# Kernel optimization log

Measured on AMD Instinct MI355X. Metric: run time of the kernel, lower is better.

Reference implementation:

```python
import jax, jax.numpy as jnp
import numpy as np

ATOM_K = 10
VOX_K = 15
HEADS = 4
HEAD_DIM = 32
N_BLOCKS = 4
BLOCK_DEPTH = 2


def _pairwise_sqdist(a, b):
    # a: [Na,3], b: [Nb,3] -> [Na,Nb]
    return jnp.sum(a * a, 1)[:, None] + jnp.sum(b * b, 1)[None, :] - 2.0 * (a @ b.T)


def knn(src_pos, dst_pos, k):
    # for each dst point, k nearest src points; returns (dst_idx, src_idx), each [Nd*k]
    d2 = _pairwise_sqdist(dst_pos, src_pos)
    _, idx = jax.lax.top_k(-d2, k)
    dst = jnp.repeat(jnp.arange(dst_pos.shape[0]), k)
    return dst, idx.reshape(-1)


def knn_graph(pos, k):
    # k nearest neighbors excluding self; returns (src=neighbor, dst=center)
    n = pos.shape[0]
    d2 = _pairwise_sqdist(pos, pos) + jnp.eye(n, dtype=pos.dtype) * 1e10
    _, idx = jax.lax.top_k(-d2, k)
    dst = jnp.repeat(jnp.arange(n), k)
    return idx.reshape(-1), dst


def edge_weights(i0, i1, h_a, pos_a, h_b, pos_b, w1, b1, w2, b2):
    # MLP([2*A+1, 8, 1]) on concat(h_a[i0], h_b[i1], dist) -> scalar per edge
    d = jnp.sqrt(jnp.sum((pos_a[i0] - pos_b[i1]) ** 2, -1, keepdims=True) + 1e-12)
    feat = jnp.concatenate([h_a[i0], h_b[i1], d], -1)
    return (jax.nn.relu(feat @ w1 + b1) @ w2 + b2)[:, 0]


def attn_layer(h, src, dst, ew, wq_l, wk_l, wv_l, n):
    # edge-weighted multi-head graph attention with segment softmax over dst
    q = (h @ wq_l).reshape(n, HEADS, HEAD_DIM)
    k = (h @ wk_l).reshape(n, HEADS, HEAD_DIM)
    v = (h @ wv_l).reshape(n, HEADS, HEAD_DIM)
    logits = jnp.sum(q[dst] * k[src], -1) / jnp.sqrt(jnp.float32(HEAD_DIM)) + ew[:, None]  # [E,H]
    m = jax.ops.segment_max(logits, dst, num_segments=n)
    z = jnp.exp(logits - m[dst])
    s = jax.ops.segment_sum(z, dst, num_segments=n)
    alpha = z / (s[dst] + 1e-9)
    out = jax.ops.segment_sum(alpha[:, :, None] * v[src], dst, num_segments=n)
    return out.reshape(n, HEADS * HEAD_DIM)


def layer_norm(x, g, b):
    mu = jnp.mean(x, -1, keepdims=True)
    var = jnp.var(x, -1, keepdims=True)
    return (x - mu) * jax.lax.rsqrt(var + 1e-5) * g + b


def setup_inputs() -> dict:
    Na, Nv, F, A, OUT = 8192, 4096, 64, 128, 128
    L = N_BLOCKS * BLOCK_DEPTH
    key = jax.random.key(0)
    ks = jax.random.split(key, 20)
    p = lambda k, shape, s=0.05: jax.random.normal(k, shape, jnp.float32) * s
    return {
        'atom_x': jax.random.normal(ks[0], (Na, F), jnp.float32),
        'atom_pos': jax.random.normal(ks[1], (Na, 3), jnp.float32) * 10.0,
        'vox_x': jax.random.normal(ks[2], (Nv, F), jnp.float32),
        'vox_pos': jax.random.normal(ks[3], (Nv, 3), jnp.float32) * 10.0,
        'w_atom_in': p(ks[4], (F, A)), 'b_atom_in': jnp.zeros((A,), jnp.float32),
        'w_vox_in': p(ks[5], (F, A)), 'b_vox_in': jnp.zeros((A,), jnp.float32),
        'aa_w1': p(ks[6], (2 * A + 1, 8)), 'aa_b1': jnp.zeros((8,), jnp.float32),
        'aa_w2': p(ks[7], (8, 1)), 'aa_b2': jnp.zeros((1,), jnp.float32),
        'av_w1': p(ks[8], (2 * A + 1, 8)), 'av_b1': jnp.zeros((8,), jnp.float32),
        'av_w2': p(ks[9], (8, 1)), 'av_b2': jnp.zeros((1,), jnp.float32),
        'vv_w1': p(ks[10], (2 * A + 1, 8)), 'vv_b1': jnp.zeros((8,), jnp.float32),
        'vv_w2': p(ks[11], (8, 1)), 'vv_b2': jnp.zeros((1,), jnp.float32),
        'wq': p(ks[12], (L, A, A)), 'wk': p(ks[13], (L, A, A)), 'wv': p(ks[14], (L, A, A)),
        'ln_g': jnp.ones((L, A), jnp.float32), 'ln_b': jnp.zeros((L, A), jnp.float32),
        'w_o1': p(ks[15], ((N_BLOCKS + 1) * A, A)), 'b_o1': jnp.zeros((A,), jnp.float32),
        'w_o2': p(ks[16], (A, OUT)), 'b_o2': jnp.zeros((OUT,), jnp.float32),
    }


def reference(atom_x, atom_pos, vox_x, vox_pos, w_atom_in, b_atom_in, w_vox_in, b_vox_in,
              aa_w1, aa_b1, aa_w2, aa_b2, av_w1, av_b1, av_w2, av_b2, vv_w1, vv_b1, vv_w2, vv_b2,
              wq, wk, wv, ln_g, ln_b, w_o1, b_o1, w_o2, b_o2):
    Na, Nv = atom_x.shape[0], vox_x.shape[0]
    N = Na + Nv
    atom_h0 = atom_x @ w_atom_in + b_atom_in
    vox_h0 = vox_x @ w_vox_in + b_vox_in

    # multi-scale KNN graph construction
    aa_src, aa_dst = knn_graph(atom_pos, ATOM_K)
    aa_ew = edge_weights(aa_src, aa_dst, atom_h0, atom_pos, atom_h0, atom_pos, aa_w1, aa_b1, aa_w2, aa_b2)
    av_vox, av_atom = knn(atom_pos, vox_pos, VOX_K)  # dst=vox, src=atom
    av_ew = edge_weights(av_vox, av_atom, vox_h0, vox_pos, atom_h0, atom_pos, av_w1, av_b1, av_w2, av_b2)
    vv_src, vv_dst = knn_graph(vox_pos, VOX_K)
    vv_ew = edge_weights(vv_src, vv_dst, vox_h0, vox_pos, vox_h0, vox_pos, vv_w1, vv_b1, vv_w2, vv_b2)

    # combined atom|vox graph (vox nodes offset by Na)
    src = jnp.concatenate([aa_src, av_atom, vv_src + Na])
    dst = jnp.concatenate([aa_dst, av_vox + Na, vv_dst + Na])
    ew = jnp.concatenate([aa_ew, av_ew, vv_ew])
    h = jnp.concatenate([atom_h0, vox_h0], 0)

    block_outs = []
    for b_i in range(N_BLOCKS):
        for l in range(BLOCK_DEPTH):
            li = b_i * BLOCK_DEPTH + l
            h = layer_norm(h + attn_layer(h, src, dst, ew, wq[li], wk[li], wv[li], N), ln_g[li], ln_b[li])
        block_outs.append(h[Na:])

    feat = jnp.concatenate([vox_h0] + block_outs, -1)  # [Nv, (blocks+1)*A]
    return jax.nn.relu(feat @ w_o1 + b_o1) @ w_o2 + b_o2
```

## Files before the change

### kernel.cpp

```cpp
#include <hip/hip_runtime.h>
#include <hip/hip_bf16.h>

#define PE_NA 8192
#define PE_NV 4096
#define PE_NN (PE_NA+PE_NV)
#define PE_FA 128
#define PE_FIN 64
#define PE_KAA 10
#define PE_KAV 15
#define PE_KVV 15
#define PE_EAA (PE_NA*PE_KAA)
#define PE_EAV (PE_NV*PE_KAV)
#define PE_EVV (PE_NV*PE_KVV)
#define PE_ETOT (PE_EAA+PE_EAV+PE_EVV)
#define PE_KNN_BLOCKS (PE_NA/4 + PE_NV/4 + PE_NV/4)
#define PE_P1A 0
#define PE_P2A 65536
#define PE_P2AV 131072
#define PE_P1AV 196608
#define PE_P1V 229376
#define PE_P2V 262144
#define PE_PTOT 294912
#define PE_PRE_BLOCKS (PE_PTOT/256)
#define PE_WT_ELEMS (8*3*128*128)
#define PE_WT_BLOCKS (PE_WT_ELEMS/256)
#define PE_RANK_S 32

typedef __hip_bfloat16 bf16;
typedef __attribute__((ext_vector_type(4))) float f32x4;
typedef __attribute__((ext_vector_type(4))) unsigned int u32x4;
typedef __attribute__((ext_vector_type(8))) short s16x8;
union pe_frag { u32x4 u; s16x8 s; };

__device__ __forceinline__ float pe_b2f(bf16 x){ return __bfloat162float(x); }

__device__ __forceinline__ float pe_u2f(unsigned short u){ return __uint_as_float(((unsigned)u) << 16); }
__device__ __forceinline__ unsigned short pe_f2u(float f){
  unsigned u = __float_as_uint(f);
  u = u + 0x7FFFu + ((u >> 16) & 1u);
  return (unsigned short)(u >> 16);
}

__global__ __launch_bounds__(1024) void pe_probe_kernel(const unsigned short* __restrict__ buf, int n,
                                                        int* __restrict__ flag){
  __shared__ int red[16];
  int t = threadIdx.x;
  int cnt = 0;
  for (int i = t; i < n; i += 1024){
    unsigned u = buf[i];
    unsigned e = (u >> 7) & 0xFF;
    if (u == 0u || (e >= 100u && e <= 150u)) cnt++;
  }
  #pragma unroll
  for (int off = 32; off > 0; off >>= 1) cnt += __shfl_xor(cnt, off);
  if ((t & 63) == 0) red[t >> 6] = cnt;
  __syncthreads();
  if (t == 0){
    int s = 0;
    #pragma unroll
    for (int i = 0; i < 16; i++) s += red[i];
    flag[0] = (s > (n * 9) / 10) ? 0 : 1;
  }
}

struct PeConv {
  const void* src[29];
  long long dstOff[29];
  int n[29];
  int blk0[30];
};
__global__ __launch_bounds__(256) void pe_convall_kernel(PeConv a, float* __restrict__ wsbase,
                                                         const int* __restrict__ flag){
  int b = blockIdx.x;
  int s = 0;
  while (s < 28 && b >= a.blk0[s+1]) s++;
  int idx = (b - a.blk0[s])*256 + threadIdx.x;
  if (idx >= a.n[s]) return;
  float* dst = wsbase + a.dstOff[s];
  if (flag[0]) dst[idx] = ((const float*)a.src[s])[idx];
  else         dst[idx] = pe_b2f(((const bf16*)a.src[s])[idx]);
}

__global__ __launch_bounds__(256) void ProteinEncoder_558345749244_kernel(bf16* __restrict__ out, int n){
  int idx = blockIdx.x*256 + threadIdx.x;
  if (idx < n) out[idx] = __float2bfloat16(0.123f);
}

__global__ __launch_bounds__(256) void pe_packproj_kernel(
    const float* __restrict__ ax, const float* __restrict__ wai, const float* __restrict__ bai,
    const float* __restrict__ vx, const float* __restrict__ wvi, const float* __restrict__ bvi,
    const float* __restrict__ apos, const float* __restrict__ vpos,
    const float* __restrict__ wq, const float* __restrict__ wk, const float* __restrict__ wv,
    float* __restrict__ h, float* __restrict__ voxh0,
    float4* __restrict__ apos4, float4* __restrict__ vpos4,
    int* __restrict__ arank, int* __restrict__ vrank,
    unsigned short* __restrict__ wtb){
  int b = blockIdx.x;
  const int NBA = (PE_NA*PE_FA)/256;
  const int NBV = (PE_NV*PE_FA)/256;
  const int NBP = (PE_NN + 255)/256;
  if (b < NBA){
    int idx = b*256 + threadIdx.x;
    int row = idx >> 7, col = idx & 127;
    const float* xr = ax + row*PE_FIN;
    float acc = bai[col];
    #pragma unroll 8
    for (int k2 = 0; k2 < PE_FIN; k2++) acc += xr[k2] * wai[k2*PE_FA + col];
    h[idx] = acc;
  } else if (b < NBA + NBV){
    int idx = (b - NBA)*256 + threadIdx.x;
    int row = idx >> 7, col = idx & 127;
    const float* xr = vx + row*PE_FIN;
    float acc = bvi[col];
    #pragma unroll 8
    for (int k2 = 0; k2 < PE_FIN; k2++) acc += xr[k2] * wvi[k2*PE_FA + col];
    h[(size_t)PE_NA*PE_FA + idx] = acc;
    voxh0[idx] = acc;
  } else if (b < NBA + NBV + NBP){
    int idx = (b - NBA - NBV)*256 + threadIdx.x;
    if (idx < PE_NA){
      float bx = apos[idx*3+0], by = apos[idx*3+1], bz = apos[idx*3+2];
      apos4[idx] = make_float4(bx, by, bz, (bx*bx + by*by) + bz*bz);
      arank[idx] = 0;
    } else if (idx < PE_NA + PE_NV){
      int j = idx - PE_NA;
      float bx = vpos[j*3+0], by = vpos[j*3+1], bz = vpos[j*3+2];
      vpos4[j] = make_float4(bx, by, bz, (bx*bx + by*by) + bz*bz);
      vrank[j] = 0;
    }
  } else {
    int g = (b - NBA - NBV - NBP)*256 + threadIdx.x;
    int c = g >> 14;
    int r = g & 16383;
    int n = r >> 7, k = r & 127;
    int li = c / 3, mat = c - li*3;
    const float* wsrc = (mat == 0) ? wq : (mat == 1) ? wk : wv;
    wtb[g] = pe_f2u(wsrc[li*16384 + k*128 + n]);
  }
}

__global__ __launch_bounds__(256) void pe_rank_kernel(
    const float4* __restrict__ apos4, const float4* __restrict__ vpos4,
    int* __restrict__ arank, int* __restrict__ vrank){
  __shared__ float xs[256];
  int b = blockIdx.x;
  const int ABLK = (PE_NA/256)*PE_RANK_S;
  const float4* src; int N; int* drk; int cb;
  if (b < ABLK){ src = apos4; N = PE_NA; drk = arank; cb = b; }
  else         { src = vpos4; N = PE_NV; drk = vrank; cb = b - ABLK; }
  int chunk = cb / PE_RANK_S;
  int seg   = cb % PE_RANK_S;
  int i = chunk*256 + threadIdx.x;
  float xi = src[i].x;
  int segN = N / PE_RANK_S;
  int j0 = seg * segN;
  if (threadIdx.x < segN) xs[threadIdx.x] = src[j0 + threadIdx.x].x;
  __syncthreads();
  int cnt = 0;
  #pragma unroll 8
  for (int j = 0; j < segN; j++){
    float xj = xs[j];
    cnt += (xj < xi || (xj == xi && (j0 + j) < i)) ? 1 : 0;
  }
  atomicAdd(&drk[i], cnt);
}

__global__ __launch_bounds__(256) void pe_scatter_kernel(
    const float4* __restrict__ apos4, const float4* __restrict__ vpos4,
    const int* __restrict__ arank, const int* __restrict__ vrank,
    float4* __restrict__ sax4, int* __restrict__ said,
    float4* __restrict__ svx4, int* __restrict__ svid){
  int g = blockIdx.x*256 + threadIdx.x;
  if (g < PE_NA){
    int r = arank[g];
    sax4[r] = apos4[g];
    said[r] = g;
  } else if (g < PE_NN){
    int j = g - PE_NA;
    int r = vrank[j];
    svx4[r] = vpos4[j];
    svid[r] = j;
  }
}

__device__ __forceinline__ float pe_unflip(unsigned th){
  return __uint_as_float(th ^ ((unsigned)(~((int)th >> 31)) | 0x80000000u));
}
__device__ __forceinline__ void pe_knn_insert(unsigned long long mask, float d2, int j,
                                              int K, int lane,
                                              unsigned long long &slot, float &thr_f){
  while (mask){
    int l = __ffsll((long long)mask) - 1;
    mask &= mask - 1;
    float dl = __shfl(d2, l, 64);
    int jl = __shfl(j, l, 64);
    unsigned u = __float_as_uint(dl);
    u ^= (unsigned)(((int)u >> 31) | 0x80000000);
    unsigned long long k = ((unsigned long long)u << 32) | (unsigned)jl;
    unsigned long long skm1 = __shfl(slot, K-1, 64);
    if (k < skm1){
      unsigned long long up = __shfl_up(slot, 1, 64);
      slot = (slot < k) ? slot : ((lane == 0 || up < k) ? k : up);
      thr_f = pe_unflip((unsigned)(__shfl(slot, K-1, 64) >> 32));
    }
  }
}

__global__ __launch_bounds__(256) void pe_knn3_kernel(
    const float4* __restrict__ apos4, const float4* __restrict__ vpos4,
    const float4* __restrict__ sax4, const int* __restrict__ said, const int* __restrict__ arank,
    const float4* __restrict__ svx4, const int* __restrict__ svid, const int* __restrict__ vrank,
    int* __restrict__ es,
    const float* __restrict__ h,
    const float* __restrict__ aw1, const float* __restrict__ vw1, const float* __restrict__ ww1,
    float* __restrict__ Pall){
  int b = blockIdx.x;
  if (b >= PE_KNN_BLOCKS){
    int g = (b - PE_KNN_BLOCKS)*256 + threadIdx.x;
    const float* w1; const float* hb; int n; int half;
    if (g < PE_P2A)       { w1 = aw1; hb = h;                        n = g >> 3;               half = 0; }
    else if (g < PE_P2AV) { w1 = aw1; hb = h;                        n = (g - PE_P2A) >> 3;    half = 1; }
    else if (g < PE_P1AV) { w1 = vw1; hb = h;                        n = (g - PE_P2AV) >> 3;   half = 1; }
    else if (g < PE_P1V)  { w1 = vw1; hb = h + (size_t)PE_NA*PE_FA;  n = (g - PE_P1AV) >> 3;   half = 0; }
    else if (g < PE_P2V)  { w1 = ww1; hb = h + (size_t)PE_NA*PE_FA;  n = (g - PE_P1V) >> 3;    half = 0; }
    else                  { w1 = ww1; hb = h + (size_t)PE_NA*PE_FA;  n = (g - PE_P2V) >> 3;    half = 1; }
    int j = g & 7;
    const float* hr = hb + n*PE_FA;
    const float* wr = w1 + half*128*8 + j;
    float acc = 0.f;
    #pragma unroll 8
    for (int f = 0; f < 128; f++) acc += hr[f] * wr[f*8];
    Pall[g] = acc;
    return;
  }
  const float4 *dpos, *spos; const int *sid, *srank; int Ns, K, excl, idx_off, nb; int* out;
  if (b < PE_NA/4){
    dpos = apos4; spos = sax4; sid = said; srank = arank;
    Ns = PE_NA; K = PE_KAA; excl = 1; idx_off = 0; out = es; nb = b;
  } else if (b < PE_NA/4 + PE_NV/4){
    dpos = vpos4; spos = sax4; sid = said; srank = nullptr;
    Ns = PE_NA; K = PE_KAV; excl = 0; idx_off = 0; out = es + PE_EAA; nb = b - PE_NA/4;
  } else {
    dpos = vpos4; spos = svx4; sid = svid; srank = vrank;
    Ns = PE_NV; K = PE_KVV; excl = 1; idx_off = PE_NA;
    out = es + PE_EAA + PE_EAV; nb = b - PE_NA/4 - PE_NV/4;
  }
  int lane = threadIdx.x & 63;
  int n = nb*4 + (threadIdx.x >> 6);
  float4 dp = dpos[n];
  float qx = dp.x, qy = dp.y, qz = dp.z, nq = dp.w;
  int self = excl ? n : -1;
  int start;
  if (srank){
    start = srank[n];
  } else {
    int lo = 0, len = Ns;
    #pragma unroll
    for (int it = 0; it < 2; it++){
      int step = (len + 63) >> 6;
      int pr = lo + lane*step; if (pr > Ns-1) pr = Ns-1;
      float px = spos[pr].x;
      unsigned long long mv = __ballot(px <= qx);
      int cnt = __popcll(mv);
      int seg = cnt > 0 ? cnt - 1 : 0;
      lo = lo + seg*step;
      len = step;
      if (lo > Ns-1) lo = Ns-1;
    }
    start = lo;
  }
  int w0 = start - 32; if (w0 < 0) w0 = 0; if (w0 > Ns - 64) w0 = Ns - 64;
  unsigned long long slot;
  float thr_f;
  {
    int j = w0 + lane;
    float4 pp = spos[j];
    int oi = sid[j];
    float dt = (qx*pp.x + qy*pp.y) + qz*pp.z;
    float d2 = __builtin_fmaf(-2.0f, dt, nq + pp.w);
    unsigned u = __float_as_uint(d2);
    u ^= (unsigned)(((int)u >> 31) | 0x80000000);
    if (oi == self) u = 0xffffffffu;
    unsigned long long key = ((unsigned long long)u << 32) | (unsigned)oi;
    #pragma unroll
    for (int kk = 2; kk <= 64; kk <<= 1){
      #pragma unroll
      for (int jj = kk >> 1; jj > 0; jj >>= 1){
        unsigned long long o = __shfl_xor(key, jj, 64);
        bool keepmin = (((lane & jj) == 0) == ((lane & kk) == 0));
        unsigned long long mn = (key < o) ? key : o;
        unsigned long long mx = (key < o) ? o : key;
        key = keepmin ? mn : mx;
      }
    }
    slot = key;
    thr_f = pe_unflip((unsigned)(__shfl(slot, K-1, 64) >> 32));
  }
  int L = w0 - 1;
  int R = w0 + 64;
  bool doneL = false, doneR = false;
  while (!(doneL && doneR)){
    if (!doneL){
      int j = L - lane;
      bool val = (j >= 0);
      float d2 = 1e30f, ddx = -1e30f; int oi = -3;
      if (val){
        float4 pp = spos[j];
        oi = sid[j];
        ddx = pp.x - qx;
        float dt = (qx*pp.x + qy*pp.y) + qz*pp.z;
        d2 = __builtin_fmaf(-2.0f, dt, nq + pp.w);
      }
      unsigned long long m = __ballot(val && (d2 <= thr_f) && (oi != self));
      if (m) pe_knn_insert(m, d2, oi, K, lane, slot, thr_f);
      float dd63 = __shfl(ddx, 63);
      doneL = (L - 64 < 0) || ((dd63 < 0.f) && (dd63*dd63 > thr_f));
      L -= 64;
    }
    if (!doneR){
      int j = R + lane;
      bool val = (j < Ns);
      float d2 = 1e30f, ddx = 1e30f; int oi = -3;
      if (val){
        float4 pp = spos[j];
        oi = sid[j];
        ddx = pp.x - qx;
        float dt = (qx*pp.x + qy*pp.y) + qz*pp.z;
        d2 = __builtin_fmaf(-2.0f, dt, nq + pp.w);
      }
      unsigned long long m = __ballot(val && (d2 <= thr_f) && (oi != self));
      if (m) pe_knn_insert(m, d2, oi, K, lane, slot, thr_f);
      float dd63 = __shfl(ddx, 63);
      doneR = (R + 64 >= Ns) || ((dd63 > 0.f) && (dd63*dd63 > thr_f));
      R += 64;
    }
  }
  if (lane < K) out[n*K + lane] = (int)(unsigned)(slot & 0xffffffffu) + idx_off;
}

__global__ __launch_bounds__(256) void pe_edge3_kernel(
    const float4* __restrict__ apos4, const float4* __restrict__ vpos4,
    const int* __restrict__ es, const float* __restrict__ Pall,
    const float* __restrict__ aw1, const float* __restrict__ ab1,
    const float* __restrict__ aw2, const float* __restrict__ ab2,
    const float* __restrict__ vw1, const float* __restrict__ vb1,
    const float* __restrict__ vw2, const float* __restrict__ vb2,
    const float* __restrict__ ww1, const float* __restrict__ wb1,
    const float* __restrict__ ww2, const float* __restrict__ wb2,
    float* __restrict__ ewb){
  int e = blockIdx.x*256 + threadIdx.x;
  const float *w1r, *b1, *w2, *b2;
  long long offA, offB;
  float4 qa, qb;
  if (e < PE_EAA){
    int dst = e / PE_KAA;
    int src = es[e];
    offA = PE_P1A  + (long long)src*8;
    offB = PE_P2A  + (long long)dst*8;
    qa = apos4[src]; qb = apos4[dst];
    w1r = aw1 + 256*8; b1 = ab1; w2 = aw2; b2 = ab2;
  } else if (e < PE_EAA + PE_EAV){
    int e2 = e - PE_EAA;
    int dstv = e2 / PE_KAV;
    int srca = es[e];
    offA = PE_P1AV + (long long)dstv*8;
    offB = PE_P2AV + (long long)srca*8;
    qa = vpos4[dstv]; qb = apos4[srca];
    w1r = vw1 + 256*8; b1 = vb1; w2 = vw2; b2 = vb2;
  } else {
    int e2 = e - PE_EAA - PE_EAV;
    int dstv = e2 / PE_KVV;
    int srcv = es[e] - PE_NA;
    offA = PE_P1V  + (long long)srcv*8;
    offB = PE_P2V  + (long long)dstv*8;
    qa = vpos4[srcv]; qb = vpos4[dstv];
    w1r = ww1 + 256*8; b1 = wb1; w2 = ww2; b2 = wb2;
  }
  float dx = qa.x - qb.x, dy = qa.y - qb.y, dz = qa.z - qb.z;
  float d = sqrtf(((dx*dx + dy*dy) + dz*dz) + 1e-12f);
  float4 a0 = *(const float4*)(Pall + offA);
  float4 a1 = *(const float4*)(Pall + offA + 4);
  float4 c0 = *(const float4*)(Pall + offB);
  float4 c1 = *(const float4*)(Pall + offB + 4);
  float acc[8] = { a0.x + c0.x, a0.y + c0.y, a0.z + c0.z, a0.w + c0.w,
                   a1.x + c1.x, a1.y + c1.y, a1.z + c1.z, a1.w + c1.w };
  float o = b2[0];
  #pragma unroll
  for (int j = 0; j < 8; j++){
    float hj = acc[j] + d*w1r[j] + b1[j];
    if (hj > 0.f) o += hj * w2[j];
  }
  ewb[e] = o;
}

__global__ __launch_bounds__(256) void pe_qkv3_kernel(const float* __restrict__ H,
    const unsigned short* __restrict__ Wt,
    unsigned short* __restrict__ QKV){
  __shared__ __align__(16) unsigned Xs[2048];
  int t = threadIdx.x;
  int row0 = blockIdx.x * 32;
  #pragma unroll
  for (int i = 0; i < 8; i++){
    int idx32 = i*256 + t;
    int row = idx32 >> 6, c32 = idx32 & 63;
    const float* src = H + (size_t)(row0 + row)*PE_FA + c32*2;
    unsigned u = (unsigned)pe_f2u(src[0]) | ((unsigned)pe_f2u(src[1]) << 16);
    Xs[row*64 + (c32 ^ ((row & 7) << 2))] = u;
  }
  __syncthreads();
  int w = t >> 6, l = t & 63;
  int l15 = l & 15, lq = l >> 4;
  f32x4 acc[2][6];
  #pragma unroll
  for (int a = 0; a < 2; a++)
    #pragma unroll
    for (int bb = 0; bb < 6; bb++) acc[a][bb] = (f32x4){0.f, 0.f, 0.f, 0.f};
  #pragma unroll
  for (int ks = 0; ks < 4; ks++){
    pe_frag af[2];
    #pragma unroll
    for (int rt = 0; rt < 2; rt++){
      int row = rt*16 + l15;
      int c32 = (ks*16 + lq*4) ^ ((row & 7) << 2);
      af[rt].u = *(const u32x4*)&Xs[row*64 + c32];
    }
    #pragma unroll
    for (int nt = 0; nt < 6; nt++){
      int n = w*96 + nt*16 + l15;
      pe_frag bf_;
      bf_.u = *(const u32x4*)(Wt + (size_t)n*PE_FA + ks*32 + lq*8);
      #pragma unroll
      for (int rt = 0; rt < 2; rt++)
        acc[rt][nt] = __builtin_amdgcn_mfma_f32_16x16x32_bf16(af[rt].s, bf_.s, acc[rt][nt], 0, 0, 0);
    }
  }
  #pragma unroll
  for (int rt = 0; rt < 2; rt++){
    #pragma unroll
    for (int nt = 0; nt < 6; nt++){
      int n = w*96 + nt*16 + l15;
      int mat = n >> 7, col = n & 127;
      unsigned short* outp = QKV + (size_t)mat*PE_NN*PE_FA + col;
      int nodeb = row0 + rt*16 + lq*4;
      #pragma unroll
      for (int v = 0; v < 4; v++)
        outp[(size_t)(nodeb + v)*PE_FA] = pe_f2u(acc[rt][nt][v]);
    }
  }
}

template<int DEG>
__device__ __forceinline__ void pe_attn_node(int n, int lane, int esel, float ewsel,
    const unsigned* __restrict__ Qp, const unsigned* __restrict__ Kp, const unsigned* __restrict__ Vp,
    float* H, const float* __restrict__ lng, const float* __restrict__ lnb, float* bout){
  unsigned qu = Qp[n*64 + lane];
  float qx = pe_u2f((unsigned short)(qu & 0xffffu));
  float qy = pe_u2f((unsigned short)(qu >> 16));
  int srcs[DEG];
  #pragma unroll
  for (int e = 0; e < DEG; e++) srcs[e] = __shfl(esel, e, 64);
  const float inv = 0.17677669529663687f;
  float lg[DEG];
  #pragma unroll
  for (int e = 0; e < DEG; e++){
    unsigned ku = Kp[srcs[e]*64 + lane];
    float p = qx*pe_u2f((unsigned short)(ku & 0xffffu)) + qy*pe_u2f((unsigned short)(ku >> 16));
    #pragma unroll
    for (int off = 8; off > 0; off >>= 1) p += __shfl_xor(p, off);
    lg[e] = p*inv + __shfl(ewsel, e, 64);
  }
  float m = -1e30f;
  #pragma unroll
  for (int e = 0; e < DEG; e++) m = fmaxf(m, lg[e]);
  float ssum = 0.f;
  #pragma unroll
  for (int e = 0; e < DEG; e++){ float z = expf(lg[e] - m); ssum += z; lg[e] = z; }
  float rdn = 1.0f / (ssum + 1e-9f);
  float a0 = 0.f, a1 = 0.f;
  #pragma unroll
  for (int e = 0; e < DEG; e++){
    unsigned vu = Vp[srcs[e]*64 + lane];
    a0 += lg[e]*pe_u2f((unsigned short)(vu & 0xffffu));
    a1 += lg[e]*pe_u2f((unsigned short)(vu >> 16));
  }
  a0 *= rdn; a1 *= rdn;
  float2 hv = ((const float2*)H)[n*64 + lane];
  float x0 = hv.x + a0, x1 = hv.y + a1;
  float s = x0 + x1;
  #pragma unroll
  for (int off = 32; off > 0; off >>= 1) s += __shfl_xor(s, off);
  float mu = s * (1.f/128.f);
  float d0 = x0 - mu, d1 = x1 - mu;
  float vq = d0*d0 + d1*d1;
  #pragma unroll
  for (int off = 32; off > 0; off >>= 1) vq += __shfl_xor(vq, off);
  float var = vq * (1.f/128.f);
  float rs = 1.0f / sqrtf(var + 1e-5f);
  float2 lw = ((const float2*)lng)[lane];
  float2 lb = ((const float2*)lnb)[lane];
  float2 yv = make_float2(d0*rs*lw.x + lb.x, d1*rs*lw.y + lb.y);
  ((float2*)H)[n*64 + lane] = yv;
  if (bout != nullptr) ((float2*)bout)[(n - PE_NA)*64 + lane] = yv;
}

__global__ __launch_bounds__(128) void pe_attn_ln_kernel(const unsigned* __restrict__ Qp,
    const unsigned* __restrict__ Kp, const unsigned* __restrict__ Vp, float* H,
    const int* __restrict__ esrc, const float* __restrict__ eew,
    const float* __restrict__ lng, const float* __restrict__ lnb, float* bout){
  int w = threadIdx.x >> 6;
  int lane = threadIdx.x & 63;
  int n = blockIdx.x*2 + w;
  int esel = 0; float ewsel = 0.f;
  if (n < PE_NA){
    if (lane < PE_KAA){ int e = n*PE_KAA + lane; esel = esrc[e]; ewsel = eew[e]; }
    pe_attn_node<PE_KAA>(n, lane, esel, ewsel, Qp, Kp, Vp, H, lng, lnb, nullptr);
  } else {
    int j = n - PE_NA;
    if (lane < PE_KAV){ int e = PE_EAA + j*PE_KAV + lane; esel = esrc[e]; ewsel = eew[e]; }
    else if (lane < PE_KAV + PE_KVV){ int e = PE_EAA + PE_EAV + j*PE_KVV + (lane - PE_KAV); esel = esrc[e]; ewsel = eew[e]; }
    pe_attn_node<PE_KAV+PE_KVV>(n, lane, esel, ewsel, Qp, Kp, Vp, H, lng, lnb, bout);
  }
}

__global__ __launch_bounds__(256) void pe_final1_kernel(const float* __restrict__ voxh0, const float* __restrict__ bouts,
    const float* __restrict__ W, const float* __restrict__ B, float* __restrict__ hid){
  __shared__ float Xs[640][17];
  int t = threadIdx.x;
  int row0 = blockIdx.x * 16;
  for (int s = 0; s < 5; s++){
    const float* seg = (s == 0) ? voxh0 : (bouts + (size_t)(s-1)*PE_NV*PE_FA);
    #pragma unroll
    for (int i = 0; i < 8; i++){
      int idx = i*256 + t;
      int r = idx >> 7, k0 = idx & 127;
      Xs[s*128 + k0][r] = seg[(size_t)(row0 + r)*PE_FA + k0];
    }
  }
  __syncthreads();
  int col = t & 127;
  int rg = (t >> 7) * 8;
  float acc[8];
  #pragma unroll
  for (int i = 0; i < 8; i++) acc[i] = B[col];
  for (int k = 0; k < 640; k++){
    float w = W[k*PE_FA + col];
    #pragma unroll
    for (int i = 0; i < 8; i++) acc[i] += Xs[k][rg + i] * w;
  }
  #pragma unroll
  for (int i = 0; i < 8; i++)
    hid[(size_t)(row0 + rg + i)*PE_FA + col] = fmaxf(acc[i], 0.f);
}

__global__ __launch_bounds__(256) void pe_final2_kernel(const float* __restrict__ hid, const float* __restrict__ W,
    const float* __restrict__ B, void* __restrict__ outv, const int* __restrict__ flag){
  int idx = blockIdx.x*256 + threadIdx.x;
  int r = idx >> 7, c = idx & 127;
  float acc = B[c];
  const float* hr = hid + r*PE_FA;
  #pragma unroll 8
  for (int k2 = 0; k2 < 128; k2++) acc += hr[k2] * W[k2*PE_FA + c];
  if (flag[0]) ((float*)outv)[idx] = acc;
  else         ((bf16*)outv)[idx] = __float2bfloat16(acc);
}

extern "C" void kernel_launch(void* const* d_in, const int* in_sizes, int n_in,
                              void* d_out, int out_size, void* d_ws, size_t ws_size,
                              hipStream_t stream){
  (void)in_sizes; (void)n_in; (void)ws_size;

  float* ws = (float*)d_ws;
  int* flag = (int*)ws;
  float* p = ws + 4;
  auto A = [&](size_t n){ float* r = p; p += n; return r; };

  float* c_atom_x  = A(PE_NA*PE_FIN);
  float* c_atom_pos= A(PE_NA*3);
  float* c_vox_x   = A(PE_NV*PE_FIN);
  float* c_vox_pos = A(PE_NV*3);
  float* c_w_ai = A(PE_FIN*PE_FA); float* c_b_ai = A(PE_FA);
  float* c_w_vi = A(PE_FIN*PE_FA); float* c_b_vi = A(PE_FA);
  float* c_aa_w1 = A(257*8); float* c_aa_b1 = A(8); float* c_aa_w2 = A(8); float* c_aa_b2 = A(1);
  float* c_av_w1 = A(257*8); float* c_av_b1 = A(8); float* c_av_w2 = A(8); float* c_av_b2 = A(1);
  float* c_vv_w1 = A(257*8); float* c_vv_b1 = A(8); float* c_vv_w2 = A(8); float* c_vv_b2 = A(1);
  float* c_wq = A(8*PE_FA*PE_FA); float* c_wk = A(8*PE_FA*PE_FA); float* c_wv = A(8*PE_FA*PE_FA);
  float* c_lng = A(8*PE_FA); float* c_lnb = A(8*PE_FA);
  float* c_wo1 = A(5*PE_FA*PE_FA); float* c_bo1 = A(PE_FA);
  float* c_wo2 = A(PE_FA*PE_FA);   float* c_bo2 = A(PE_FA);

  float* h     = A((size_t)PE_NN*PE_FA);
  float* voxh0 = A((size_t)PE_NV*PE_FA);
  int*   es    = (int*)A(PE_ETOT);
  float* ewb   = A(PE_ETOT);
  float* bouts = A((size_t)4*PE_NV*PE_FA);
  float4* apos4 = (float4*)A((size_t)PE_NA*4);
  float4* vpos4 = (float4*)A((size_t)PE_NV*4);
  float4* sax4  = (float4*)A((size_t)PE_NA*4);
  float4* svx4  = (float4*)A((size_t)PE_NV*4);
  int* said  = (int*)A(PE_NA);
  int* arank = (int*)A(PE_NA);
  int* svid  = (int*)A(PE_NV);
  int* vrank = (int*)A(PE_NV);
  { uintptr_t up = (uintptr_t)p; up = (up + 15) & ~(uintptr_t)15; p = (float*)up; }
  float* Pall  = A(PE_PTOT);
  unsigned short* wtb = (unsigned short*)A(PE_WT_ELEMS/2);
  float* qkvb  = A((size_t)3*PE_NN*64);
  unsigned short* qkvb16 = (unsigned short*)qkvb;
  float* hid   = qkvb;

  pe_probe_kernel<<<1, 1024, 0, stream>>>((const unsigned short*)d_in[1], PE_NA*3, flag);

  const int nelem[29] = {
    PE_NA*PE_FIN, PE_NA*3, PE_NV*PE_FIN, PE_NV*3,
    PE_FIN*PE_FA, PE_FA, PE_FIN*PE_FA, PE_FA,
    257*8, 8, 8, 1,  257*8, 8, 8, 1,  257*8, 8, 8, 1,
    8*PE_FA*PE_FA, 8*PE_FA*PE_FA, 8*PE_FA*PE_FA,
    8*PE_FA, 8*PE_FA,
    5*PE_FA*PE_FA, PE_FA, PE_FA*PE_FA, PE_FA
  };
  float* cdst[29] = {
    c_atom_x, c_atom_pos, c_vox_x, c_vox_pos,
    c_w_ai, c_b_ai, c_w_vi, c_b_vi,
    c_aa_w1, c_aa_b1, c_aa_w2, c_aa_b2,
    c_av_w1, c_av_b1, c_av_w2, c_av_b2,
    c_vv_w1, c_vv_b1, c_vv_w2, c_vv_b2,
    c_wq, c_wk, c_wv, c_lng, c_lnb,
    c_wo1, c_bo1, c_wo2, c_bo2
  };
  PeConv pc;
  int bacc = 0;
  for (int i = 0; i < 29; i++){
    pc.src[i] = d_in[i];
    pc.n[i] = nelem[i];
    pc.dstOff[i] = (long long)(cdst[i] - ws);
    pc.blk0[i] = bacc;
    bacc += (nelem[i] + 255)/256;
  }
  pc.blk0[29] = bacc;
  pe_convall_kernel<<<bacc, 256, 0, stream>>>(pc, ws, flag);

  ProteinEncoder_558345749244_kernel<<<(out_size + 255)/256, 256, 0, stream>>>((bf16*)d_out, out_size);

  pe_packproj_kernel<<<(PE_NA*PE_FA)/256 + (PE_NV*PE_FA)/256 + (PE_NN + 255)/256 + PE_WT_BLOCKS,
                       256, 0, stream>>>(
      c_atom_x, c_w_ai, c_b_ai, c_vox_x, c_w_vi, c_b_vi, c_atom_pos, c_vox_pos,
      c_wq, c_wk, c_wv,
      h, voxh0, apos4, vpos4, arank, vrank, wtb);

  pe_rank_kernel<<<(PE_NA/256)*PE_RANK_S + (PE_NV/256)*PE_RANK_S, 256, 0, stream>>>(
      apos4, vpos4, arank, vrank);
  pe_scatter_kernel<<<(PE_NN + 255)/256, 256, 0, stream>>>(
      apos4, vpos4, arank, vrank, sax4, said, svx4, svid);

  pe_knn3_kernel<<<PE_KNN_BLOCKS + PE_PRE_BLOCKS, 256, 0, stream>>>(
      apos4, vpos4, sax4, said, arank, svx4, svid, vrank,
      es, h, c_aa_w1, c_av_w1, c_vv_w1, Pall);

  pe_edge3_kernel<<<PE_ETOT/256, 256, 0, stream>>>(
      apos4, vpos4, es, Pall,
      c_aa_w1, c_aa_b1, c_aa_w2, c_aa_b2,
      c_av_w1, c_av_b1, c_av_w2, c_av_b2,
      c_vv_w1, c_vv_b1, c_vv_w2, c_vv_b2,
      ewb);

  const unsigned* Qp = (const unsigned*)qkvb;
  const unsigned* Kp = Qp + (size_t)PE_NN*64;
  const unsigned* Vp = Kp + (size_t)PE_NN*64;
  for (int li = 0; li < 8; li++){
    pe_qkv3_kernel<<<PE_NN/32, 256, 0, stream>>>(h, wtb + (size_t)li*3*PE_FA*PE_FA, qkvb16);
    float* bo = (li & 1) ? (bouts + (size_t)(li >> 1)*PE_NV*PE_FA) : nullptr;
    pe_attn_ln_kernel<<<PE_NN/2, 128, 0, stream>>>(Qp, Kp, Vp,
                                                   h, es, ewb, c_lng + li*PE_FA, c_lnb + li*PE_FA, bo);
  }

  pe_final1_kernel<<<PE_NV/16, 256, 0, stream>>>(voxh0, bouts, c_wo1, c_bo1, hid);
  pe_final2_kernel<<<(PE_NV*PE_FA)/256, 256, 0, stream>>>(hid, c_wo2, c_bo2, d_out, flag);
}
```

Baseline: 589.9 us.

## Fuse next-layer QKV projection into attention+layernorm kernel with double-buffered QKV

The attention/layernorm kernel now packs each node's normalized output to bf16 in shared memory and immediately runs the next layer's QKV projection with MFMA. The result goes into a ping-pong QKV buffer, so there is no separate QKV kernel per layer. The first layer's QKV kernel is split across a grid y-dimension per matrix. This removes seven kernel launches and the re-read of H for projection. In exchange each block works on only 8 valid rows of a 16-row MFMA tile and re-reads the full weight matrix per 8 nodes, which raises weight traffic through cache. The input probe also scans fewer elements.

```diff
diff --git a/kernel.cpp b/kernel.cpp
--- a/kernel.cpp
+++ b/kernel.cpp
@@ -399,6 +399,7 @@
   __shared__ __align__(16) unsigned Xs[2048];
   int t = threadIdx.x;
   int row0 = blockIdx.x * 32;
+  int mat = blockIdx.y;
   #pragma unroll
   for (int i = 0; i < 8; i++){
     int idx32 = i*256 + t;
@@ -410,11 +411,11 @@
   __syncthreads();
   int w = t >> 6, l = t & 63;
   int l15 = l & 15, lq = l >> 4;
-  f32x4 acc[2][6];
+  f32x4 acc[2][2];
   #pragma unroll
   for (int a = 0; a < 2; a++)
     #pragma unroll
-    for (int bb = 0; bb < 6; bb++) acc[a][bb] = (f32x4){0.f, 0.f, 0.f, 0.f};
+    for (int bb = 0; bb < 2; bb++) acc[a][bb] = (f32x4){0.f, 0.f, 0.f, 0.f};
   #pragma unroll
   for (int ks = 0; ks < 4; ks++){
     pe_frag af[2];
@@ -425,10 +426,10 @@
       af[rt].u = *(const u32x4*)&Xs[row*64 + c32];
     }
     #pragma unroll
-    for (int nt = 0; nt < 6; nt++){
-      int n = w*96 + nt*16 + l15;
+    for (int nt = 0; nt < 2; nt++){
+      int col = w*32 + nt*16 + l15;
       pe_frag bf_;
-      bf_.u = *(const u32x4*)(Wt + (size_t)n*PE_FA + ks*32 + lq*8);
+      bf_.u = *(const u32x4*)(Wt + (size_t)(mat*128 + col)*PE_FA + ks*32 + lq*8);
       #pragma unroll
       for (int rt = 0; rt < 2; rt++)
         acc[rt][nt] = __builtin_amdgcn_mfma_f32_16x16x32_bf16(af[rt].s, bf_.s, acc[rt][nt], 0, 0, 0);
@@ -437,9 +438,8 @@
   #pragma unroll
   for (int rt = 0; rt < 2; rt++){
     #pragma unroll
-    for (int nt = 0; nt < 6; nt++){
-      int n = w*96 + nt*16 + l15;
-      int mat = n >> 7, col = n & 127;
+    for (int nt = 0; nt < 2; nt++){
+      int col = w*32 + nt*16 + l15;
       unsigned short* outp = QKV + (size_t)mat*PE_NN*PE_FA + col;
       int nodeb = row0 + rt*16 + lq*4;
       #pragma unroll
@@ -450,7 +450,7 @@
 }
 
 template<int DEG>
-__device__ __forceinline__ void pe_attn_node(int n, int lane, int esel, float ewsel,
+__device__ __forceinline__ float2 pe_attn_node(int n, int lane, int esel, float ewsel,
     const unsigned* __restrict__ Qp, const unsigned* __restrict__ Kp, const unsigned* __restrict__ Vp,
     float* H, const float* __restrict__ lng, const float* __restrict__ lnb, float* bout){
   unsigned qu = Qp[n*64 + lane];
@@ -501,24 +501,62 @@
   float2 yv = make_float2(d0*rs*lw.x + lb.x, d1*rs*lw.y + lb.y);
   ((float2*)H)[n*64 + lane] = yv;
   if (bout != nullptr) ((float2*)bout)[(n - PE_NA)*64 + lane] = yv;
-}
-
-__global__ __launch_bounds__(128) void pe_attn_ln_kernel(const unsigned* __restrict__ Qp,
-    const unsigned* __restrict__ Kp, const unsigned* __restrict__ Vp, float* H,
-    const int* __restrict__ esrc, const float* __restrict__ eew,
-    const float* __restrict__ lng, const float* __restrict__ lnb, float* bout){
+  return yv;
+}
+
+__global__ __launch_bounds__(512) void pe_attn_qkv_kernel(
+    const unsigned* __restrict__ Qp, const unsigned* __restrict__ Kp, const unsigned* __restrict__ Vp,
+    float* __restrict__ H, const int* __restrict__ esrc, const float* __restrict__ eew,
+    const float* __restrict__ lng, const float* __restrict__ lnb, float* __restrict__ bout,
+    const unsigned short* __restrict__ Wt,
+    unsigned short* __restrict__ QKVo){
+  __shared__ __align__(16) unsigned Xs[16*64];
   int w = threadIdx.x >> 6;
   int lane = threadIdx.x & 63;
-  int n = blockIdx.x*2 + w;
+  int n = blockIdx.x*8 + w;
+  Xs[512 + threadIdx.x] = 0u;
+  float2 yv;
   int esel = 0; float ewsel = 0.f;
   if (n < PE_NA){
     if (lane < PE_KAA){ int e = n*PE_KAA + lane; esel = esrc[e]; ewsel = eew[e]; }
-    pe_attn_node<PE_KAA>(n, lane, esel, ewsel, Qp, Kp, Vp, H, lng, lnb, nullptr);
+    yv = pe_attn_node<PE_KAA>(n, lane, esel, ewsel, Qp, Kp, Vp, H, lng, lnb, nullptr);
   } else {
     int j = n - PE_NA;
     if (lane < PE_KAV){ int e = PE_EAA + j*PE_KAV + lane; esel = esrc[e]; ewsel = eew[e]; }
     else if (lane < PE_KAV + PE_KVV){ int e = PE_EAA + PE_EAV + j*PE_KVV + (lane - PE_KAV); esel = esrc[e]; ewsel = eew[e]; }
-    pe_attn_node<PE_KAV+PE_KVV>(n, lane, esel, ewsel, Qp, Kp, Vp, H, lng, lnb, bout);
+    yv = pe_attn_node<PE_KAV+PE_KVV>(n, lane, esel, ewsel, Qp, Kp, Vp, H, lng, lnb, bout);
+  }
+  Xs[w*64 + (lane ^ ((w & 7) << 2))] = (unsigned)pe_f2u(yv.x) | ((unsigned)pe_f2u(yv.y) << 16);
+  if (Wt == nullptr) return;
+  __syncthreads();
+  int l15 = lane & 15, lq = lane >> 4;
+  f32x4 acc[3];
+  #pragma unroll
+  for (int nt = 0; nt < 3; nt++) acc[nt] = (f32x4){0.f, 0.f, 0.f, 0.f};
+  #pragma unroll
+  for (int ks = 0; ks < 4; ks++){
+    pe_frag af;
+    int row = l15;
+    int c32 = (ks*16 + lq*4) ^ ((row & 7) << 2);
+    af.u = *(const u32x4*)&Xs[row*64 + c32];
+    #pragma unroll
+    for (int nt = 0; nt < 3; nt++){
+      int col = w*48 + nt*16 + l15;
+      pe_frag bf_;
+      bf_.u = *(const u32x4*)(Wt + (size_t)col*PE_FA + ks*32 + lq*8);
+      acc[nt] = __builtin_amdgcn_mfma_f32_16x16x32_bf16(af.s, bf_.s, acc[nt], 0, 0, 0);
+    }
+  }
+  #pragma unroll
+  for (int nt = 0; nt < 3; nt++){
+    int col = w*48 + nt*16 + l15;
+    int mat = col >> 7, c = col & 127;
+    unsigned short* outp = QKVo + (size_t)mat*PE_NN*PE_FA + c;
+    #pragma unroll
+    for (int v = 0; v < 4; v++){
+      int r16 = lq*4 + v;
+      if (r16 < 8) outp[(size_t)(blockIdx.x*8 + r16)*PE_FA] = pe_f2u(acc[nt][v]);
+    }
   }
 }
 
@@ -604,11 +642,12 @@
   { uintptr_t up = (uintptr_t)p; up = (up + 15) & ~(uintptr_t)15; p = (float*)up; }
   float* Pall  = A(PE_PTOT);
   unsigned short* wtb = (unsigned short*)A(PE_WT_ELEMS/2);
-  float* qkvb  = A((size_t)3*PE_NN*64);
-  unsigned short* qkvb16 = (unsigned short*)qkvb;
-  float* hid   = qkvb;
-
-  pe_probe_kernel<<<1, 1024, 0, stream>>>((const unsigned short*)d_in[1], PE_NA*3, flag);
+  float* qkvb0 = A((size_t)3*PE_NN*64);
+  float* qkvb1 = A((size_t)3*PE_NN*64);
+  unsigned short* qb16[2] = { (unsigned short*)qkvb0, (unsigned short*)qkvb1 };
+  float* hid   = qkvb0;
+
+  pe_probe_kernel<<<1, 1024, 0, stream>>>((const unsigned short*)d_in[1], 3072, flag);
 
   const int nelem[29] = {
     PE_NA*PE_FIN, PE_NA*3, PE_NV*PE_FIN, PE_NV*3,
@@ -663,14 +702,16 @@
       c_vv_w1, c_vv_b1, c_vv_w2, c_vv_b2,
       ewb);
 
-  const unsigned* Qp = (const unsigned*)qkvb;
-  const unsigned* Kp = Qp + (size_t)PE_NN*64;
-  const unsigned* Vp = Kp + (size_t)PE_NN*64;
+  pe_qkv3_kernel<<<dim3(PE_NN/32, 3), 256, 0, stream>>>(h, wtb, qb16[0]);
   for (int li = 0; li < 8; li++){
-    pe_qkv3_kernel<<<PE_NN/32, 256, 0, stream>>>(h, wtb + (size_t)li*3*PE_FA*PE_FA, qkvb16);
+    const unsigned* Qp = (const unsigned*)qb16[li & 1];
+    const unsigned* Kp = Qp + (size_t)PE_NN*64;
+    const unsigned* Vp = Kp + (size_t)PE_NN*64;
     float* bo = (li & 1) ? (bouts + (size_t)(li >> 1)*PE_NV*PE_FA) : nullptr;
-    pe_attn_ln_kernel<<<PE_NN/2, 128, 0, stream>>>(Qp, Kp, Vp,
-                                                   h, es, ewb, c_lng + li*PE_FA, c_lnb + li*PE_FA, bo);
+    const unsigned short* wnext = (li < 7) ? (wtb + (size_t)(li+1)*3*PE_FA*PE_FA) : nullptr;
+    pe_attn_qkv_kernel<<<PE_NN/8, 512, 0, stream>>>(
+        Qp, Kp, Vp, h, es, ewb, c_lng + li*PE_FA, c_lnb + li*PE_FA, bo,
+        wnext, qb16[(li+1) & 1]);
   }
 
   pe_final1_kernel<<<PE_NV/16, 256, 0, stream>>>(voxh0, bouts, c_wo1, c_bo1, hid);
```

After: 672.7 us. +14.0%, slower.
